# Optimization experiments

Measured on AMD Instinct MI355X. Metric: run time of the kernel, lower is better.

Reference implementation:

```python
import jax, jax.numpy as jnp
import numpy as np


def setup_inputs() -> dict:
    key = jax.random.key(0)
    k1, k2, k3, k4 = jax.random.split(key, 4)
    Q = jax.random.normal(k1, (32, 32, 128), dtype=jnp.float32)
    D = jax.random.normal(k2, (512, 180, 128), dtype=jnp.float32)
    q_mask = jax.random.randint(k3, (32, 32), 0, 2, dtype=jnp.int32)
    d_mask = jax.random.randint(k4, (512, 180), 0, 2, dtype=jnp.int32)
    return {"Q": Q, "D": D, "q_mask": q_mask, "d_mask": d_mask}


def reference(Q, D, q_mask, d_mask):
    # ColBERT MaxSim late-interaction scoring (ColBERT_List_qa.score)
    # Q: [q, m, h], D: [d, n, h]; masks zero out padding token embeddings.
    Qm = Q * q_mask.astype(Q.dtype)[..., None]              # [q, m, h]
    Dm = D * d_mask.astype(D.dtype)[..., None]              # [d, n, h]
    sim = jnp.einsum("qmh,dnh->qdmn", Qm, Dm)               # [q, d, m, n]
    scores = sim.max(axis=-1).sum(axis=-1)                  # max over doc tokens n, sum over query tokens m -> [q, d]
    return scores
```

## Files before the change

kernel.cpp:

```cpp
#include <hip/hip_runtime.h>
#include <hip/hip_bf16.h>

typedef __attribute__((ext_vector_type(8))) short short8;
typedef __attribute__((ext_vector_type(4))) float f32x4;

#define NQ 32
#define NM 32
#define NH 128
#define ND 512
#define NN 180
#define NTMAX 12
#define MTILES 64
#define LSTR 136

#define QFRAG_BYTES (MTILES * 4 * 64 * 16)
#define QSTART_OFF  QFRAG_BYTES
#define T2_OFF      (QSTART_OFF + 33 * 4)

static __device__ __forceinline__ unsigned short f2bf(float x) {
  __hip_bfloat16 h = __float2bfloat16(x);
  return __builtin_bit_cast(unsigned short, h);
}

static __device__ __forceinline__ uint4 pack8(float4 a, float4 b) {
  unsigned int x = (unsigned)f2bf(a.x) | ((unsigned)f2bf(a.y) << 16);
  unsigned int y = (unsigned)f2bf(a.z) | ((unsigned)f2bf(a.w) << 16);
  unsigned int z = (unsigned)f2bf(b.x) | ((unsigned)f2bf(b.y) << 16);
  unsigned int u = (unsigned)f2bf(b.z) | ((unsigned)f2bf(b.w) << 16);
  return make_uint4(x, y, z, u);
}

__global__ __launch_bounds__(1024) void prep_q_compact(
    const float* __restrict__ Q, const int* __restrict__ qmask,
    unsigned short* __restrict__ Qb, int* __restrict__ qstart_g,
    int* __restrict__ t2_g) {
  __shared__ unsigned short src_tok[NQ * NM];
  __shared__ int wtot16[16], base16[16], total_s;
  const int tid = threadIdx.x;
  const int lane = tid & 63;
  const int wv = tid >> 6;

  const int flag = qmask[tid];
  unsigned long long bal = __ballot(flag != 0);
  int pre = __popcll(bal & ((1ull << lane) - 1ull));
  if (lane == 63) wtot16[wv] = pre + (flag ? 1 : 0);
  __syncthreads();
  if (tid == 0) {
    int run = 0;
    #pragma unroll
    for (int i = 0; i < 16; ++i) { base16[i] = run; run += wtot16[i]; }
    total_s = run;
  }
  __syncthreads();
  const int pos = base16[wv] + pre;
  if (flag) src_tok[pos] = (unsigned short)tid;
  if (blockIdx.x == 0 && (tid & 31) == 0) qstart_g[tid >> 5] = pos;
  __syncthreads();
  const int total = total_s;
  if (blockIdx.x == 0 && tid == 0) {
    qstart_g[32] = total;
    int T = (total + 15) >> 4;
    t2_g[0] = (T + 1) >> 1;
  }

  if (tid < 256) {
    int s = blockIdx.x * 256 + tid;
    int t2 = s >> 8, ks = (s >> 6) & 3, ln = s & 63;
    int col = t2 * 16 + (ln & 15);
    int kk = ks * 32 + (ln >> 4) * 8;
    uint4 o = make_uint4(0u, 0u, 0u, 0u);
    if (col < total) {
      int tok = src_tok[col];
      const float* src = Q + tok * NH + kk;
      float4 a = *reinterpret_cast<const float4*>(src);
      float4 b = *reinterpret_cast<const float4*>(src + 4);
      o = pack8(a, b);
    }
    reinterpret_cast<uint4*>(Qb)[s] = o;
  }
}

__global__ __launch_bounds__(512, 4) void fused_maxsim(
    const float* __restrict__ D, const int* __restrict__ dmask,
    const unsigned short* __restrict__ Qb, const int* __restrict__ qstart_g,
    const int* __restrict__ t2_g, float* __restrict__ out) {
  __shared__ unsigned short Dlds[192 * LSTR];
  __shared__ float colmax[MTILES * 16];
  __shared__ unsigned short mapinv[192];
  __shared__ int wtot[4];
  const int d = blockIdx.x;
  const int tid = threadIdx.x;
  const int lane = tid & 63;
  const int w = tid >> 6;
  const float NEG = -__builtin_inff();

  int flag = 0, pre = 0;
  if (tid < NN) flag = dmask[d * NN + tid];
  if (tid < 192) {
    unsigned long long bal = __ballot(flag != 0);
    pre = __popcll(bal & ((1ull << lane) - 1ull));
    if (lane == 63) wtot[w] = pre + (flag ? 1 : 0);
  }
  __syncthreads();
  const int cnt = wtot[0] + wtot[1] + wtot[2];
  if (tid < 192 && flag) {
    int base = (w >= 1 ? wtot[0] : 0) + (w >= 2 ? wtot[1] : 0);
    mapinv[pre + base] = (unsigned short)tid;
  }
  __syncthreads();

  const int ntc = (cnt + 15) >> 4;
  {
    const int rg = tid >> 5;
    const int c4 = tid & 31;
    const int nrows = ntc * 16;
    #pragma unroll 2
    for (int base = 0; base < nrows; base += 16) {
      int dr = base + rg;
      uint2 o = make_uint2(0u, 0u);
      if (dr < cnt) {
        int sr = mapinv[dr];
        float4 v = reinterpret_cast<const float4*>(D)[(size_t)(d * NN + sr) * 32 + c4];
        o.x = (unsigned)f2bf(v.x) | ((unsigned)f2bf(v.y) << 16);
        o.y = (unsigned)f2bf(v.z) | ((unsigned)f2bf(v.w) << 16);
      }
      *reinterpret_cast<uint2*>(&Dlds[dr * LSTR + c4 * 4]) = o;
    }
  }
  __syncthreads();

  const int bl = lane & 15;
  const int bg = lane >> 4;
  const int T2 = t2_g[0];

  #pragma unroll 1
  for (int tp = w; tp < T2; tp += 8) {
    const int t0 = tp * 2;

    short8 Qf0[4], Qf1[4];
    #pragma unroll
    for (int ks = 0; ks < 4; ++ks) {
      Qf0[ks] = *reinterpret_cast<const short8*>(
          reinterpret_cast<const char*>(Qb) +
          (((t0 * 4 + ks) << 10) + (lane << 4)));
      Qf1[ks] = *reinterpret_cast<const short8*>(
          reinterpret_cast<const char*>(Qb) +
          ((((t0 + 1) * 4 + ks) << 10) + (lane << 4)));
    }

    float run0 = NEG, run1 = NEG;

    #pragma unroll 2
    for (int nt = 0; nt < ntc; ++nt) {
      short8 Da[4];
      #pragma unroll
      for (int ks = 0; ks < 4; ++ks)
        Da[ks] = *reinterpret_cast<const short8*>(
            &Dlds[(nt * 16 + bl) * LSTR + ks * 32 + bg * 8]);

      f32x4 acc0 = {0.f, 0.f, 0.f, 0.f};
      f32x4 acc1 = acc0;
      #pragma unroll
      for (int ks = 0; ks < 4; ++ks) {
        acc0 = __builtin_amdgcn_mfma_f32_16x16x32_bf16(Da[ks], Qf0[ks], acc0, 0, 0, 0);
        acc1 = __builtin_amdgcn_mfma_f32_16x16x32_bf16(Da[ks], Qf1[ks], acc1, 0, 0, 0);
      }

      if (nt * 16 + 16 > cnt) {
        const int rlim = cnt - nt * 16 - bg * 4;
        float v0 = NEG, v1 = NEG;
        #pragma unroll
        for (int j = 0; j < 4; ++j) {
          v0 = fmaxf(v0, (j < rlim) ? acc0[j] : NEG);
          v1 = fmaxf(v1, (j < rlim) ? acc1[j] : NEG);
        }
        run0 = fmaxf(run0, v0);
        run1 = fmaxf(run1, v1);
      } else {
        run0 = fmaxf(run0, fmaxf(fmaxf(acc0[0], acc0[1]), fmaxf(acc0[2], acc0[3])));
        run1 = fmaxf(run1, fmaxf(fmaxf(acc1[0], acc1[1]), fmaxf(acc1[2], acc1[3])));
      }
    }

    if (cnt < NN) {
      run0 = fmaxf(run0, 0.f);
      run1 = fmaxf(run1, 0.f);
    }

    run0 = fmaxf(run0, __shfl_xor(run0, 16));
    run0 = fmaxf(run0, __shfl_xor(run0, 32));
    run1 = fmaxf(run1, __shfl_xor(run1, 16));
    run1 = fmaxf(run1, __shfl_xor(run1, 32));

    if (lane < 16) {
      colmax[t0 * 16 + lane] = run0;
      colmax[(t0 + 1) * 16 + lane] = run1;
    }
  }
  __syncthreads();

  if (tid < NQ) {
    const int s0 = qstart_g[tid];
    const int s1 = qstart_g[tid + 1];
    float s = 0.f;
    for (int i = s0; i < s1; ++i) s += colmax[i];
    out[tid * ND + d] = s;
  }
}

extern "C" void kernel_launch(void* const* d_in, const int* in_sizes, int n_in,
                              void* d_out, int out_size, void* d_ws, size_t ws_size,
                              hipStream_t stream) {
  const float* Q = (const float*)d_in[0];
  const float* D = (const float*)d_in[1];
  const int* qmask = (const int*)d_in[2];
  const int* dmask = (const int*)d_in[3];
  float* out = (float*)d_out;

  unsigned short* Qb = (unsigned short*)d_ws;
  int* qstart_g = (int*)((char*)d_ws + QSTART_OFF);
  int* t2_g = (int*)((char*)d_ws + T2_OFF);

  prep_q_compact<<<64, 1024, 0, stream>>>(Q, qmask, Qb, qstart_g, t2_g);
  fused_maxsim<<<ND, 512, 0, stream>>>(D, dmask, Qb, qstart_g, t2_g, out);
}
```

Baseline: 21.64 us.

## Prefetch first Q fragments before D staging and shrink prep kernel blocks

The main kernel now issues the global loads for each wave's first pair of Q tiles before staging the document tile into LDS, so their latency overlaps the D conversion loop. It also raises the unroll of that staging loop. The prep kernel drops from 1024 to 256 threads per block, with each thread handling four mask entries and one fewer barrier. The cost is higher register pressure from the prefetched fragments, and the early loads are unguarded, so they may read unused workspace when a wave has no tile.

```diff
diff --git a/kernel.cpp b/kernel.cpp
--- a/kernel.cpp
+++ b/kernel.cpp
@@ -30,40 +30,56 @@
   return make_uint4(x, y, z, u);
 }
 
-__global__ __launch_bounds__(1024) void prep_q_compact(
+__global__ __launch_bounds__(256) void prep_q_compact(
     const float* __restrict__ Q, const int* __restrict__ qmask,
     unsigned short* __restrict__ Qb, int* __restrict__ qstart_g,
     int* __restrict__ t2_g) {
   __shared__ unsigned short src_tok[NQ * NM];
-  __shared__ int wtot16[16], base16[16], total_s;
+  __shared__ int rtot[16];
   const int tid = threadIdx.x;
   const int lane = tid & 63;
   const int wv = tid >> 6;
 
-  const int flag = qmask[tid];
-  unsigned long long bal = __ballot(flag != 0);
-  int pre = __popcll(bal & ((1ull << lane) - 1ull));
-  if (lane == 63) wtot16[wv] = pre + (flag ? 1 : 0);
-  __syncthreads();
-  if (tid == 0) {
+  int flags[4], pres[4];
+  #pragma unroll
+  for (int r = 0; r < 4; ++r) {
+    int idx = r * 256 + tid;
+    int f = qmask[idx];
+    unsigned long long bal = __ballot(f != 0);
+    int pre = __popcll(bal & ((1ull << lane) - 1ull));
+    if (lane == 63) rtot[r * 4 + wv] = pre + (f ? 1 : 0);
+    flags[r] = f;
+    pres[r] = pre;
+  }
+  __syncthreads();
+  int total = 0;
+  int chunkbase[4];
+  {
     int run = 0;
     #pragma unroll
-    for (int i = 0; i < 16; ++i) { base16[i] = run; run += wtot16[i]; }
-    total_s = run;
-  }
-  __syncthreads();
-  const int pos = base16[wv] + pre;
-  if (flag) src_tok[pos] = (unsigned short)tid;
-  if (blockIdx.x == 0 && (tid & 31) == 0) qstart_g[tid >> 5] = pos;
-  __syncthreads();
-  const int total = total_s;
+    for (int r = 0; r < 4; ++r) {
+      chunkbase[r] = run + ((wv >= 1) ? rtot[r * 4 + 0] : 0) +
+                           ((wv >= 2) ? rtot[r * 4 + 1] : 0) +
+                           ((wv >= 3) ? rtot[r * 4 + 2] : 0);
+      run += rtot[r * 4 + 0] + rtot[r * 4 + 1] + rtot[r * 4 + 2] + rtot[r * 4 + 3];
+    }
+    total = run;
+  }
+  #pragma unroll
+  for (int r = 0; r < 4; ++r) {
+    int idx = r * 256 + tid;
+    int pos = chunkbase[r] + pres[r];
+    if (flags[r]) src_tok[pos] = (unsigned short)idx;
+    if (blockIdx.x == 0 && (idx & 31) == 0) qstart_g[idx >> 5] = pos;
+  }
+  __syncthreads();
   if (blockIdx.x == 0 && tid == 0) {
     qstart_g[32] = total;
     int T = (total + 15) >> 4;
     t2_g[0] = (T + 1) >> 1;
   }
 
-  if (tid < 256) {
+  {
     int s = blockIdx.x * 256 + tid;
     int t2 = s >> 8, ks = (s >> 6) & 3, ln = s & 63;
     int col = t2 * 16 + (ln & 15);
@@ -109,12 +125,29 @@
   }
   __syncthreads();
 
+  const int T2 = t2_g[0];
+
+  short8 Qp0[4], Qp1[4];
+  const bool hasFirst = (w < T2);
+  {
+    const int t0 = w * 2;
+    #pragma unroll
+    for (int ks = 0; ks < 4; ++ks) {
+      Qp0[ks] = *reinterpret_cast<const short8*>(
+          reinterpret_cast<const char*>(Qb) +
+          (((t0 * 4 + ks) << 10) + (lane << 4)));
+      Qp1[ks] = *reinterpret_cast<const short8*>(
+          reinterpret_cast<const char*>(Qb) +
+          ((((t0 + 1) * 4 + ks) << 10) + (lane << 4)));
+    }
+  }
+
   const int ntc = (cnt + 15) >> 4;
   {
     const int rg = tid >> 5;
     const int c4 = tid & 31;
     const int nrows = ntc * 16;
-    #pragma unroll 2
+    #pragma unroll 4
     for (int base = 0; base < nrows; base += 16) {
       int dr = base + rg;
       uint2 o = make_uint2(0u, 0u);
@@ -131,21 +164,25 @@
 
   const int bl = lane & 15;
   const int bg = lane >> 4;
-  const int T2 = t2_g[0];
 
   #pragma unroll 1
   for (int tp = w; tp < T2; tp += 8) {
     const int t0 = tp * 2;
 
     short8 Qf0[4], Qf1[4];
-    #pragma unroll
-    for (int ks = 0; ks < 4; ++ks) {
-      Qf0[ks] = *reinterpret_cast<const short8*>(
-          reinterpret_cast<const char*>(Qb) +
-          (((t0 * 4 + ks) << 10) + (lane << 4)));
-      Qf1[ks] = *reinterpret_cast<const short8*>(
-          reinterpret_cast<const char*>(Qb) +
-          ((((t0 + 1) * 4 + ks) << 10) + (lane << 4)));
+    if (tp == w) {
+      #pragma unroll
+      for (int ks = 0; ks < 4; ++ks) { Qf0[ks] = Qp0[ks]; Qf1[ks] = Qp1[ks]; }
+    } else {
+      #pragma unroll
+      for (int ks = 0; ks < 4; ++ks) {
+        Qf0[ks] = *reinterpret_cast<const short8*>(
+            reinterpret_cast<const char*>(Qb) +
+            (((t0 * 4 + ks) << 10) + (lane << 4)));
+        Qf1[ks] = *reinterpret_cast<const short8*>(
+            reinterpret_cast<const char*>(Qb) +
+            ((((t0 + 1) * 4 + ks) << 10) + (lane << 4)));
+      }
     }
 
     float run0 = NEG, run1 = NEG;
@@ -221,6 +258,6 @@
   int* qstart_g = (int*)((char*)d_ws + QSTART_OFF);
   int* t2_g = (int*)((char*)d_ws + T2_OFF);
 
-  prep_q_compact<<<64, 1024, 0, stream>>>(Q, qmask, Qb, qstart_g, t2_g);
+  prep_q_compact<<<64, 256, 0, stream>>>(Q, qmask, Qb, qstart_g, t2_g);
   fused_maxsim<<<ND, 512, 0, stream>>>(D, dmask, Qb, qstart_g, t2_g, out);
 }
```

After: 21.61 us. No clear change (-0.1%).
